# Kernel optimization log

Hardware: AMD Instinct MI355X
Metric: run time of the kernel (lower is better)

The kernel has to match this reference:

```python
import jax, jax.numpy as jnp
import numpy as np

EPS = 1e-6
H = 8        # num_heads
DH = 64      # head dim = embed_dim // num_heads
LN_EPS = 1e-5


def _layernorm(x, g, b):
    m = jnp.mean(x, axis=-1, keepdims=True)
    v = jnp.mean(jnp.square(x - m), axis=-1, keepdims=True)
    return (x - m) / jnp.sqrt(v + LN_EPS) * g + b


def _flow_attention(x, Wq, bq, Wk, bk, Wv, bv, Wo, bo):
    # Non-causal Flow-Attention (Flowformer): kernelized sigmoid Q/K,
    # flow-conservation sink/source normalization, linear-attention kv trick.
    B, L, D = x.shape
    S = L
    q = jax.nn.sigmoid((x @ Wq + bq).reshape(B, L, H, DH).transpose(0, 2, 1, 3))  # bhld
    k = jax.nn.sigmoid((x @ Wk + bk).reshape(B, S, H, DH).transpose(0, 2, 1, 3))
    v = (x @ Wv + bv).reshape(B, S, H, DH).transpose(0, 2, 1, 3)

    sink_incoming = 1.0 / jnp.einsum('nhld,nhd->nhl', q + EPS, k.sum(axis=2) + EPS)
    source_outgoing = 1.0 / jnp.einsum('nhld,nhd->nhl', k + EPS, q.sum(axis=2) + EPS)
    conserved_sink = jnp.einsum('nhld,nhd->nhl', q + EPS,
                                (k * source_outgoing[..., None]).sum(axis=2) + EPS)
    conserved_source = jnp.einsum('nhld,nhd->nhl', k + EPS,
                                  (q * sink_incoming[..., None]).sum(axis=2) + EPS)
    conserved_source = jnp.clip(conserved_source, -1.0, 1.0)
    sink_allocation = jax.nn.sigmoid(conserved_sink * (float(L) / float(S)))
    source_competition = jax.nn.softmax(conserved_source, axis=-1) * float(S)

    # linear attention: kv = k^T (v * comp), out = (q * sink_in) kv
    kv = jnp.einsum('nhld,nhlm->nhdm', k, v * source_competition[..., None])
    o = jnp.einsum('nhld,nhdm->nhlm', q * sink_incoming[..., None], kv)
    o = o * sink_allocation[..., None]
    o = o.transpose(0, 2, 1, 3).reshape(B, L, D)
    return o @ Wo + bo


def setup_inputs() -> dict:
    key = jax.random.key(0)
    ks = jax.random.split(key, 16)
    B, L, D, F = 2, 16384, 512, 2048
    s = 0.02
    inp = {
        'x': jax.random.normal(ks[0], (B, L, D), dtype=jnp.float32),
        'Wq': jax.random.normal(ks[1], (D, D), dtype=jnp.float32) * s,
        'bq': jnp.zeros((D,), jnp.float32),
        'Wk': jax.random.normal(ks[2], (D, D), dtype=jnp.float32) * s,
        'bk': jnp.zeros((D,), jnp.float32),
        'Wv': jax.random.normal(ks[3], (D, D), dtype=jnp.float32) * s,
        'bv': jnp.zeros((D,), jnp.float32),
        'Wo': jax.random.normal(ks[4], (D, D), dtype=jnp.float32) * s,
        'bo': jnp.zeros((D,), jnp.float32),
        'W1': jax.random.normal(ks[5], (D, F), dtype=jnp.float32) * s,
        'b1': jnp.zeros((F,), jnp.float32),
        'W2': jax.random.normal(ks[6], (F, D), dtype=jnp.float32) * s,
        'b2': jnp.zeros((D,), jnp.float32),
        'g1': jnp.ones((D,), jnp.float32),
        'be1': jnp.zeros((D,), jnp.float32),
        'g2': jnp.ones((D,), jnp.float32),
        'be2': jnp.zeros((D,), jnp.float32),
    }
    return inp


def reference(x, Wq, bq, Wk, bk, Wv, bv, Wo, bo, W1, b1, W2, b2, g1, be1, g2, be2):
    # norm_first FlowformerLayer. NOTE: original _sa_block returns
    # dropout(attn(x))[0, :, :] -> [L, D], broadcast-added over batch (faithful).
    sa = _flow_attention(_layernorm(x, g1, be1), Wq, bq, Wk, bk, Wv, bv, Wo, bo)[0]
    x = x + sa  # [B,L,D] + [L,D]
    h = _layernorm(x, g2, be2)
    h = jax.nn.gelu(h @ W1 + b1, approximate=False) @ W2 + b2
    return x + h
```

## Files before the change

### kernel.cpp

```cpp
#include <hip/hip_runtime.h>
#include <hip/hip_bf16.h>
#include <cstdint>
#include <cstddef>


#define L_SEQ 16384
#define EPSF 1e-6f

typedef __bf16 b16x8 __attribute__((ext_vector_type(8)));
typedef __bf16 b16x4 __attribute__((ext_vector_type(4)));
typedef float  f32x4 __attribute__((ext_vector_type(4)));

#define FENCE() asm volatile("" ::: "memory")
#define BARF()  { FENCE(); __builtin_amdgcn_s_barrier(); FENCE(); }
#define WAITV(n) asm volatile("s_waitcnt vmcnt(" #n ")" ::: "memory")

__device__ __forceinline__ void gload16(const void* g, void* l) {
  __builtin_amdgcn_global_load_lds((const __attribute__((address_space(1))) void*)g,
                                   (__attribute__((address_space(3))) void*)l, 16, 0, 0);
}

__device__ __forceinline__ float sigmoidf_(float x) { return 1.f / (1.f + __expf(-x)); }

__global__ __launch_bounds__(256) void convT(const float* __restrict__ src,
                                             __bf16* __restrict__ dst, int K, int N) {
  __shared__ float tile[32][33];
  const int k0 = blockIdx.y * 32, n0 = blockIdx.x * 32;
  const int tx = threadIdx.x & 31, ty = threadIdx.x >> 5;
#pragma unroll
  for (int i = 0; i < 32; i += 8) tile[ty + i][tx] = src[(size_t)(k0 + ty + i) * N + n0 + tx];
  __syncthreads();
#pragma unroll
  for (int i = 0; i < 32; i += 8)
    dst[(size_t)(n0 + ty + i) * K + k0 + tx] = (__bf16)tile[tx][ty + i];
}

__global__ __launch_bounds__(256) void biascat_k(const float* __restrict__ bq,
                                                 const float* __restrict__ bk,
                                                 const float* __restrict__ bv,
                                                 float* __restrict__ bc) {
  int i = blockIdx.x * 256 + threadIdx.x;
  bc[i] = (i < 512) ? bq[i] : (i < 1024) ? bk[i - 512] : bv[i - 1024];
}

__global__ __launch_bounds__(256) void zero_k(float* __restrict__ p, int n) {
  int i = blockIdx.x * 256 + threadIdx.x;
  if (i < n) p[i] = 0.f;
}

__global__ __launch_bounds__(128) void ln_rows(const float* __restrict__ x,
                                               const float* __restrict__ g,
                                               const float* __restrict__ be,
                                               __bf16* __restrict__ out) {
  const int row = blockIdx.x, t = threadIdx.x;
  const float4 xv = reinterpret_cast<const float4*>(x + (size_t)row * 512)[t];
  float s = xv.x + xv.y + xv.z + xv.w;
  float s2 = xv.x * xv.x + xv.y * xv.y + xv.z * xv.z + xv.w * xv.w;
#pragma unroll
  for (int off = 32; off > 0; off >>= 1) { s += __shfl_down(s, off); s2 += __shfl_down(s2, off); }
  __shared__ float red[4];
  if ((t & 63) == 0) { red[(t >> 6) * 2] = s; red[(t >> 6) * 2 + 1] = s2; }
  __syncthreads();
  const float S = red[0] + red[2], S2 = red[1] + red[3];
  const float mean = S * (1.f / 512.f);
  const float var = S2 * (1.f / 512.f) - mean * mean;
  const float inv = rsqrtf(var + 1e-5f);
  const float4 gv = reinterpret_cast<const float4*>(g)[t];
  const float4 bv = reinterpret_cast<const float4*>(be)[t];
  b16x4 o;
  o[0] = (__bf16)((xv.x - mean) * inv * gv.x + bv.x);
  o[1] = (__bf16)((xv.y - mean) * inv * gv.y + bv.y);
  o[2] = (__bf16)((xv.z - mean) * inv * gv.z + bv.z);
  o[3] = (__bf16)((xv.w - mean) * inv * gv.w + bv.w);
  reinterpret_cast<b16x4*>(out + (size_t)row * 512)[t] = o;
}

__global__ __launch_bounds__(128) void x2ln2_k(const float* __restrict__ x,
                                               const float* __restrict__ sa0,
                                               const float* __restrict__ sa1,
                                               const float* __restrict__ bo,
                                               const float* __restrict__ g,
                                               const float* __restrict__ be,
                                               float* __restrict__ xout,
                                               __bf16* __restrict__ lnout) {
  const int row = blockIdx.x, t = threadIdx.x;
  const int l = row & (L_SEQ - 1);
  float4 xv = reinterpret_cast<const float4*>(x + (size_t)row * 512)[t];
  const float4 s0 = reinterpret_cast<const float4*>(sa0 + (size_t)l * 512)[t];
  const float4 s1 = reinterpret_cast<const float4*>(sa1 + (size_t)l * 512)[t];
  const float4 bb = reinterpret_cast<const float4*>(bo)[t];
  xv.x += s0.x + s1.x + bb.x; xv.y += s0.y + s1.y + bb.y;
  xv.z += s0.z + s1.z + bb.z; xv.w += s0.w + s1.w + bb.w;
  reinterpret_cast<float4*>(xout + (size_t)row * 512)[t] = xv;
  float s = xv.x + xv.y + xv.z + xv.w;
  float s2 = xv.x * xv.x + xv.y * xv.y + xv.z * xv.z + xv.w * xv.w;
#pragma unroll
  for (int off = 32; off > 0; off >>= 1) { s += __shfl_down(s, off); s2 += __shfl_down(s2, off); }
  __shared__ float red[4];
  if ((t & 63) == 0) { red[(t >> 6) * 2] = s; red[(t >> 6) * 2 + 1] = s2; }
  __syncthreads();
  const float S = red[0] + red[2], S2 = red[1] + red[3];
  const float mean = S * (1.f / 512.f);
  const float var = S2 * (1.f / 512.f) - mean * mean;
  const float inv = rsqrtf(var + 1e-5f);
  const float4 gv = reinterpret_cast<const float4*>(g)[t];
  const float4 bv = reinterpret_cast<const float4*>(be)[t];
  b16x4 o;
  o[0] = (__bf16)((xv.x - mean) * inv * gv.x + bv.x);
  o[1] = (__bf16)((xv.y - mean) * inv * gv.y + bv.y);
  o[2] = (__bf16)((xv.z - mean) * inv * gv.z + bv.z);
  o[3] = (__bf16)((xv.w - mean) * inv * gv.w + bv.w);
  reinterpret_cast<b16x4*>(lnout + (size_t)row * 512)[t] = o;
}

template <int EPI, int KSPL>
__global__ __launch_bounds__(256, 4) void gemm128(const __bf16* __restrict__ A,
                                                  const __bf16* __restrict__ Bt,
                                                  const int M, const int N, const int K,
                                                  const float* __restrict__ bias,
                                                  float* __restrict__ f0,
                                                  __bf16* __restrict__ h0,
                                                  __bf16* __restrict__ h1,
                                                  float* __restrict__ f1,
                                                  float* __restrict__ f2) {
  __shared__ alignas(16) __bf16 lds[16384];

  if constexpr (KSPL) {
    const int z = blockIdx.y;
    A += (size_t)z * (K >> 1);
    Bt += (size_t)z * (K >> 1);
    f0 += (size_t)z * ((size_t)M * N);
  }
  const int nt = KSPL ? (K >> 6) : (K >> 5);

  const int nwg = gridDim.x;
  const int orig = blockIdx.x;
  const int cpx = nwg >> 3;
  const int wg = (orig & 7) * cpx + (orig >> 3);
  const int gx = N >> 7;
  const int bm = (wg / gx) << 7;
  const int bn = (wg % gx) << 7;

  const int t = threadIdx.x;
  const int w = t >> 6, lane = t & 63;
  const int wr = w >> 1, wc = w & 1;
  const int fr = lane & 15;
  const int kb = lane >> 4;

  const __bf16* As = A + (size_t)(bm + (t >> 2)) * K + (t & 3) * 8;
  const __bf16* Bs = Bt + (size_t)(bn + (t >> 2)) * K + (t & 3) * 8;

  f32x4 acc[4][4] = {};

  auto STG = [&](int s) {
    const int sel = (s & 1) * 4096;
    const __bf16* ap = As + (s << 5);
    const __bf16* bp = Bs + (s << 5);
    gload16(ap, &lds[sel + t * 8]);
    gload16(ap + (size_t)64 * K, &lds[sel + 2048 + t * 8]);
    gload16(bp, &lds[8192 + sel + t * 8]);
    gload16(bp + (size_t)64 * K, &lds[8192 + sel + 2048 + t * 8]);
  };

  STG(0);
  WAITV(0);
  BARF();

  for (int s = 0; s < nt; s++) {
    if (s + 1 < nt) STG(s + 1);
    const int ab = (s & 1) * 4096 + (wr * 64 + fr) * 32 + kb * 8;
    const int bb2 = 8192 + (s & 1) * 4096 + (wc * 64 + fr) * 32 + kb * 8;
    b16x8 av[4], bv[4];
#pragma unroll
    for (int m = 0; m < 4; m++)
      av[m] = *reinterpret_cast<const b16x8*>(&lds[ab + m * 512]);
#pragma unroll
    for (int n = 0; n < 4; n++)
      bv[n] = *reinterpret_cast<const b16x8*>(&lds[bb2 + n * 512]);
#pragma unroll
    for (int m = 0; m < 4; m++)
#pragma unroll
      for (int n = 0; n < 4; n++)
        acc[m][n] = __builtin_amdgcn_mfma_f32_16x16x32_bf16(av[m], bv[n], acc[m][n], 0, 0, 0);
    WAITV(0);
    BARF();
  }

  const int r0 = kb * 4;
  const int cc = fr;
  if constexpr (EPI == 0) {
    const int which = bn >> 9;
    float cs[4] = {0.f, 0.f, 0.f, 0.f};
#pragma unroll
    for (int m = 0; m < 4; m++) {
#pragma unroll
      for (int n = 0; n < 4; n++) {
        const int col = bn + wc * 64 + n * 16 + cc;
        const int c2 = col & 511;
#pragma unroll
        for (int r = 0; r < 4; r++) {
          const int row = bm + wr * 64 + m * 16 + r0 + r;
          float val = acc[m][n][r] + bias[col];
          if (which < 2) {
            val = sigmoidf_(val);
            cs[n] += val;
            ((which == 0) ? h0 : h1)[(size_t)row * 512 + c2] = (__bf16)val;
          } else {
            f0[(size_t)row * 512 + c2] = val;
          }
        }
      }
    }
    if (which < 2) {
      float* sums = (which == 0) ? f1 : f2;
#pragma unroll
      for (int n = 0; n < 4; n++) {
        float s = cs[n];
        s += __shfl_xor(s, 16);
        s += __shfl_xor(s, 32);
        if (kb == 0) atomicAdd(&sums[(bn & 511) + wc * 64 + n * 16 + cc], s);
      }
    }
  } else {
#pragma unroll
    for (int m = 0; m < 4; m++) {
#pragma unroll
      for (int n = 0; n < 4; n++) {
        const int col = bn + wc * 64 + n * 16 + cc;
#pragma unroll
        for (int r = 0; r < 4; r++) {
          const int row = bm + wr * 64 + m * 16 + r0 + r;
          float val = acc[m][n][r];
          if constexpr (EPI == 1) {
            f0[(size_t)row * N + col] = val;
          } else if constexpr (EPI == 2) {
            const float xg = val + bias[col];
            const float gel = 0.5f * xg * (1.f + erff(xg * 0.70710678118f));
            h0[(size_t)row * N + col] = (__bf16)gel;
          } else {
            const size_t idx = (size_t)row * N + col;
            f0[idx] = f0[idx] + val + bias[col];
          }
        }
      }
    }
  }
}

__global__ __launch_bounds__(256) void attn_pass1(const __bf16* __restrict__ q,
                                                  const __bf16* __restrict__ k,
                                                  const float* __restrict__ qsum,
                                                  const float* __restrict__ ksum,
                                                  float* __restrict__ si_out,
                                                  float* __restrict__ qkpart) {
  __shared__ float lsQ[512], lsK[512];
  const int t = threadIdx.x, lane = t & 63, wv = t >> 6;
  const int c0 = lane * 8;
  lsQ[t] = 0.f; lsQ[t + 256] = 0.f;
  lsK[t] = 0.f; lsK[t + 256] = 0.f;
  __syncthreads();
  float qs[8], ks[8];
#pragma unroll
  for (int j = 0; j < 8; j++) {
    qs[j] = qsum[c0 + j] + EPSF;
    ks[j] = ksum[c0 + j] + EPSF;
  }
  const int h = lane >> 3;
  float qacc[8] = {}, kacc[8] = {};
#pragma unroll 1
  for (int i = 0; i < 8; i++) {
    const int l = blockIdx.x * 32 + wv * 8 + i;
    const b16x8 q8 = *reinterpret_cast<const b16x8*>(q + (size_t)l * 512 + c0);
    const b16x8 k8 = *reinterpret_cast<const b16x8*>(k + (size_t)l * 512 + c0);
    float qf[8], kf[8];
    float p1 = 0.f, p2 = 0.f;
#pragma unroll
    for (int j = 0; j < 8; j++) {
      qf[j] = (float)q8[j]; kf[j] = (float)k8[j];
      p1 += (qf[j] + EPSF) * ks[j];
      p2 += (kf[j] + EPSF) * qs[j];
    }
    p1 += __shfl_xor(p1, 1); p2 += __shfl_xor(p2, 1);
    p1 += __shfl_xor(p1, 2); p2 += __shfl_xor(p2, 2);
    p1 += __shfl_xor(p1, 4); p2 += __shfl_xor(p2, 4);
    const float siv = 1.f / p1, sov = 1.f / p2;
    if ((lane & 7) == 0) si_out[h * L_SEQ + l] = siv;
#pragma unroll
    for (int j = 0; j < 8; j++) { qacc[j] += qf[j] * siv; kacc[j] += kf[j] * sov; }
  }
#pragma unroll
  for (int j = 0; j < 8; j++) {
    atomicAdd(&lsQ[c0 + j], qacc[j]);
    atomicAdd(&lsK[c0 + j], kacc[j]);
  }
  __syncthreads();
  float* qp = qkpart + (size_t)blockIdx.x * 1024;
  qp[t] = lsQ[t];
  qp[t + 256] = lsQ[t + 256];
  qp[t + 512] = lsK[t];
  qp[t + 768] = lsK[t + 256];
}

__global__ __launch_bounds__(256) void reduce_qk(const float* __restrict__ qkpart,
                                                 float* __restrict__ outv) {
  const int i = blockIdx.x * 256 + threadIdx.x;
  float s = 0.f;
#pragma unroll 4
  for (int b = 0; b < 512; b++) s += qkpart[(size_t)b * 1024 + i];
  outv[i] = s;
}

__global__ __launch_bounds__(256) void kv_part(const __bf16* __restrict__ k,
                                               const float* __restrict__ v,
                                               const float* __restrict__ qsi,
                                               float* __restrict__ kvpart,
                                               float* __restrict__ separt) {
  const int h = blockIdx.y, bx = blockIdx.x, t = threadIdx.x;
  __shared__ float lsK[64 * 68];
  __shared__ float lsV[64 * 68];
  __shared__ float lsRed[256];
  const int r = t >> 2, cq = (t & 3) * 16;
  float qv[16];
#pragma unroll
  for (int j = 0; j < 16; j++) qv[j] = qsi[h * 64 + cq + j] + EPSF;
  const int d = t & 63, mg = t >> 6;
  f32x4 acc4[4] = {};
  float seloc = 0.f;
#pragma unroll 1
  for (int sc = 0; sc < 4; sc++) {
    const int l = bx * 256 + sc * 64 + r;
    __syncthreads();
    const b16x8 k8a = *reinterpret_cast<const b16x8*>(k + (size_t)l * 512 + h * 64 + cq);
    const b16x8 k8b = *reinterpret_cast<const b16x8*>(k + (size_t)l * 512 + h * 64 + cq + 8);
    f32x4 v4[4];
#pragma unroll
    for (int jj = 0; jj < 4; jj++)
      v4[jj] = *reinterpret_cast<const f32x4*>(v + (size_t)l * 512 + h * 64 + cq + jj * 4);
    float kf[16];
#pragma unroll
    for (int j = 0; j < 8; j++) { kf[j] = (float)k8a[j]; kf[8 + j] = (float)k8b[j]; }
    float p = 0.f;
#pragma unroll
    for (int j = 0; j < 16; j++) p += (kf[j] + EPSF) * qv[j];
    p += __shfl_xor(p, 1);
    p += __shfl_xor(p, 2);
    p = fminf(fmaxf(p, -1.f), 1.f);
    const float ce = __expf(p);
    if ((t & 3) == 0) seloc += ce;
#pragma unroll
    for (int j = 0; j < 16; j++) lsK[r * 68 + cq + j] = kf[j];
#pragma unroll
    for (int jj = 0; jj < 4; jj++)
      *reinterpret_cast<f32x4*>(&lsV[r * 68 + cq + jj * 4]) = v4[jj] * ce;
    __syncthreads();
    for (int rr = 0; rr < 64; rr++) {
      const float kd = lsK[rr * 68 + d];
      const f32x4* lv = reinterpret_cast<const f32x4*>(&lsV[rr * 68 + mg * 16]);
#pragma unroll
      for (int jj = 0; jj < 4; jj++) acc4[jj] += lv[jj] * kd;
    }
  }
  float* kp = kvpart + ((size_t)h * 64 + bx) * 4096;
#pragma unroll
  for (int jj = 0; jj < 4; jj++)
    *reinterpret_cast<f32x4*>(&kp[d * 64 + mg * 16 + jj * 4]) = acc4[jj];
  lsRed[t] = ((t & 3) == 0) ? seloc : 0.f;
  __syncthreads();
  for (int s2 = 128; s2 > 0; s2 >>= 1) {
    if (t < s2) lsRed[t] += lsRed[t + s2];
    __syncthreads();
  }
  if (t == 0) separt[h * 64 + bx] = lsRed[0];
}

__global__ __launch_bounds__(256) void kv_reduce(const float* __restrict__ kvpart,
                                                 const float* __restrict__ separt,
                                                 float* __restrict__ kvout,
                                                 float* __restrict__ sumexp) {
  const int h = blockIdx.y, t = threadIdx.x;
  const int i = blockIdx.x * 256 + t;
  float s = 0.f;
#pragma unroll 4
  for (int b = 0; b < 64; b++) s += kvpart[((size_t)h * 64 + b) * 4096 + i];
  kvout[h * 4096 + i] = s;
  if (blockIdx.x == 0 && t < 64) {
    float e = separt[h * 64 + t];
#pragma unroll
    for (int off2 = 32; off2 > 0; off2 >>= 1) e += __shfl_down(e, off2);
    if (t == 0) sumexp[h] = e;
  }
}

__global__ __launch_bounds__(256) void o_kernel(const __bf16* __restrict__ q,
                                                const float* __restrict__ kvin,
                                                const float* __restrict__ si,
                                                const float* __restrict__ kso,
                                                const float* __restrict__ sumexp,
                                                __bf16* __restrict__ o) {
  const int h = blockIdx.y;
  const int l0 = blockIdx.x * 32;
  const int t = threadIdx.x;
  __shared__ float lsKV[64 * 64];
  __shared__ float lsQ[32 * 65];
  __shared__ float lsF[32];
  const float Sfac = (float)L_SEQ / sumexp[h];
#pragma unroll
  for (int j = 0; j < 16; j++) lsKV[t + j * 256] = kvin[h * 4096 + t + j * 256];
  const int r = t >> 3, c8 = (t & 7) * 8;
  float ksov[8];
#pragma unroll
  for (int j = 0; j < 8; j++) ksov[j] = kso[h * 64 + c8 + j] + EPSF;
  const b16x8 q8 = *reinterpret_cast<const b16x8*>(q + (size_t)(l0 + r) * 512 + h * 64 + c8);
  float p = 0.f;
#pragma unroll
  for (int j = 0; j < 8; j++) {
    const float qf = (float)q8[j];
    lsQ[r * 65 + c8 + j] = qf;
    p += (qf + EPSF) * ksov[j];
  }
  p += __shfl_xor(p, 1);
  p += __shfl_xor(p, 2);
  p += __shfl_xor(p, 4);
  if ((t & 7) == 0) lsF[r] = sigmoidf_(p) * si[h * L_SEQ + l0 + r] * Sfac;
  __syncthreads();
  const int m = t & 63, rg = t >> 6;
#pragma unroll 1
  for (int i = 0; i < 8; i++) {
    const int rr = rg + i * 4;
    float a = 0.f;
#pragma unroll
    for (int dd = 0; dd < 64; dd++) a += lsQ[rr * 65 + dd] * lsKV[dd * 64 + m];
    o[(size_t)(l0 + rr) * 512 + h * 64 + m] = (__bf16)(a * lsF[rr]);
  }
}

extern "C" void kernel_launch(void* const* d_in, const int* in_sizes, int n_in,
                              void* d_out, int out_size, void* d_ws, size_t ws_size,
                              hipStream_t stream) {
  const float* x  = (const float*)d_in[0];
  const float* Wq = (const float*)d_in[1];
  const float* bq = (const float*)d_in[2];
  const float* Wk = (const float*)d_in[3];
  const float* bk = (const float*)d_in[4];
  const float* Wv = (const float*)d_in[5];
  const float* bv = (const float*)d_in[6];
  const float* Wo = (const float*)d_in[7];
  const float* bo = (const float*)d_in[8];
  const float* W1 = (const float*)d_in[9];
  const float* b1 = (const float*)d_in[10];
  const float* W2 = (const float*)d_in[11];
  const float* b2 = (const float*)d_in[12];
  const float* g1 = (const float*)d_in[13];
  const float* be1 = (const float*)d_in[14];
  const float* g2 = (const float*)d_in[15];
  const float* be2 = (const float*)d_in[16];
  float* out = (float*)d_out;

  char* ws = (char*)d_ws;
  size_t off = 0;
  auto alloc = [&](size_t bytes) -> char* {
    char* p = ws + off;
    off += (bytes + 255) & ~(size_t)255;
    return p;
  };

  char* regA = alloc(134217728);
  __bf16* ln1  = (__bf16*)regA;
  __bf16* qb16 = (__bf16*)(regA + 16777216);
  __bf16* kb16 = (__bf16*)(regA + 33554432);
  float*  vb   = (float*)(regA + 50331648);
  __bf16* ob   = (__bf16*)(regA + 83886080);
  float*  sa   = (float*)regA;
  __bf16* act  = (__bf16*)regA;

  __bf16* ln2 = (__bf16*)alloc((size_t)32768 * 512 * 2);
  __bf16* Wqkvt = (__bf16*)alloc((size_t)1536 * 512 * 2);
  __bf16* Wot = (__bf16*)alloc((size_t)512 * 512 * 2);
  __bf16* W1t = (__bf16*)alloc((size_t)2048 * 512 * 2);
  __bf16* W2t = (__bf16*)alloc((size_t)512 * 2048 * 2);
  float* biascat = (float*)alloc(1536 * 4);
  float* si = (float*)alloc((size_t)8 * L_SEQ * 4);
  float* stats = (float*)alloc(34880 * 4);
  float* qsum = stats;
  float* ksum = stats + 512;
  float* qsi = stats + 1024;
  float* kso = stats + 1536;
  float* sumexp = stats + 2048;
  float* kvbuf = stats + 2112;
  float* kvpart = (float*)alloc((size_t)8 * 64 * 4096 * 4);
  float* separt = (float*)alloc(512 * 4);
  float* qkpart = (float*)alloc((size_t)512 * 1024 * 4);

  convT<<<dim3(16, 16), 256, 0, stream>>>(Wq, Wqkvt, 512, 512);
  convT<<<dim3(16, 16), 256, 0, stream>>>(Wk, Wqkvt + (size_t)512 * 512, 512, 512);
  convT<<<dim3(16, 16), 256, 0, stream>>>(Wv, Wqkvt + (size_t)1024 * 512, 512, 512);
  convT<<<dim3(16, 16), 256, 0, stream>>>(Wo, Wot, 512, 512);
  convT<<<dim3(64, 16), 256, 0, stream>>>(W1, W1t, 512, 2048);
  convT<<<dim3(16, 64), 256, 0, stream>>>(W2, W2t, 2048, 512);
  biascat_k<<<6, 256, 0, stream>>>(bq, bk, bv, biascat);
  zero_k<<<(2112 + 255) / 256, 256, 0, stream>>>(stats, 2112);

  ln_rows<<<L_SEQ, 128, 0, stream>>>(x, g1, be1, ln1);
  gemm128<0, 0><<<1536, 256, 0, stream>>>(ln1, Wqkvt, L_SEQ, 1536, 512,
                                          biascat, vb, qb16, kb16, qsum, ksum);

  attn_pass1<<<512, 256, 0, stream>>>(qb16, kb16, qsum, ksum, si, qkpart);
  reduce_qk<<<4, 256, 0, stream>>>(qkpart, qsi);
  kv_part<<<dim3(64, 8), 256, 0, stream>>>(kb16, vb, qsi, kvpart, separt);
  kv_reduce<<<dim3(16, 8), 256, 0, stream>>>(kvpart, separt, kvbuf, sumexp);
  o_kernel<<<dim3(L_SEQ / 32, 8), 256, 0, stream>>>(qb16, kvbuf, si, kso, sumexp, ob);

  gemm128<1, 1><<<dim3(512, 2), 256, 0, stream>>>(ob, Wot, L_SEQ, 512, 512,
                                                  nullptr, sa, nullptr, nullptr,
                                                  nullptr, nullptr);

  x2ln2_k<<<2 * L_SEQ, 128, 0, stream>>>(x, sa, sa + (size_t)L_SEQ * 512, bo,
                                         g2, be2, out, ln2);

  gemm128<2, 0><<<4096, 256, 0, stream>>>(ln2, W1t, 2 * L_SEQ, 2048, 512,
                                          b1, nullptr, act, nullptr, nullptr, nullptr);
  gemm128<3, 0><<<1024, 256, 0, stream>>>(act, W2t, 2 * L_SEQ, 512, 2048,
                                          b2, out, nullptr, nullptr, nullptr, nullptr);
}
```

Measured before the change: 514.0 us.

## Store V projection in bf16 and merge weight-prep kernels into one launch

Merges the six weight transpose/convert launches, the bias concat and the stats zeroing into a single prep kernel that dispatches on block index. This cuts launch overhead. It also stores the V projection as bf16 instead of fp32, halving the V write in the QKV GEMM epilogue and the V read in kv_part. The trade-off is lower precision on V before the kv accumulation, plus scalar LDS stores in kv_part where f32x4 stores were used before.

```diff
diff --git a/kernel.cpp b/kernel.cpp
--- a/kernel.cpp
+++ b/kernel.cpp
@@ -22,10 +22,39 @@
 
 __device__ __forceinline__ float sigmoidf_(float x) { return 1.f / (1.f + __expf(-x)); }
 
-__global__ __launch_bounds__(256) void convT(const float* __restrict__ src,
-                                             __bf16* __restrict__ dst, int K, int N) {
+__global__ __launch_bounds__(256) void prep_k(const float* __restrict__ Wq,
+                                              const float* __restrict__ Wk,
+                                              const float* __restrict__ Wv,
+                                              const float* __restrict__ Wo,
+                                              const float* __restrict__ W1,
+                                              const float* __restrict__ W2,
+                                              const float* __restrict__ bq,
+                                              const float* __restrict__ bk,
+                                              const float* __restrict__ bv,
+                                              __bf16* __restrict__ Wqkvt,
+                                              __bf16* __restrict__ Wot,
+                                              __bf16* __restrict__ W1t,
+                                              __bf16* __restrict__ W2t,
+                                              float* __restrict__ biascat,
+                                              float* __restrict__ zstats) {
+  const int b = blockIdx.x;
+  if (b >= 3072) {
+    const int i = (b - 3072) * 256 + threadIdx.x;
+    if (i < 1536) biascat[i] = (i < 512) ? bq[i] : (i < 1024) ? bk[i - 512] : bv[i - 1024];
+    else if (i < 1536 + 2112) zstats[i - 1536] = 0.f;
+    return;
+  }
+  const float* src;
+  __bf16* dst;
+  int K, N, bx, by;
+  if (b < 256)       { src = Wq; dst = Wqkvt;                      K = 512;  N = 512;  const int r = b;        bx = r & 15; by = r >> 4; }
+  else if (b < 512)  { src = Wk; dst = Wqkvt + (size_t)512 * 512;  K = 512;  N = 512;  const int r = b - 256;  bx = r & 15; by = r >> 4; }
+  else if (b < 768)  { src = Wv; dst = Wqkvt + (size_t)1024 * 512; K = 512;  N = 512;  const int r = b - 512;  bx = r & 15; by = r >> 4; }
+  else if (b < 1024) { src = Wo; dst = Wot;                        K = 512;  N = 512;  const int r = b - 768;  bx = r & 15; by = r >> 4; }
+  else if (b < 2048) { src = W1; dst = W1t;                        K = 512;  N = 2048; const int r = b - 1024; bx = r & 63; by = r >> 6; }
+  else               { src = W2; dst = W2t;                        K = 2048; N = 512;  const int r = b - 2048; bx = r & 15; by = r >> 4; }
   __shared__ float tile[32][33];
-  const int k0 = blockIdx.y * 32, n0 = blockIdx.x * 32;
+  const int k0 = by * 32, n0 = bx * 32;
   const int tx = threadIdx.x & 31, ty = threadIdx.x >> 5;
 #pragma unroll
   for (int i = 0; i < 32; i += 8) tile[ty + i][tx] = src[(size_t)(k0 + ty + i) * N + n0 + tx];
@@ -33,19 +62,6 @@
 #pragma unroll
   for (int i = 0; i < 32; i += 8)
     dst[(size_t)(n0 + ty + i) * K + k0 + tx] = (__bf16)tile[tx][ty + i];
-}
-
-__global__ __launch_bounds__(256) void biascat_k(const float* __restrict__ bq,
-                                                 const float* __restrict__ bk,
-                                                 const float* __restrict__ bv,
-                                                 float* __restrict__ bc) {
-  int i = blockIdx.x * 256 + threadIdx.x;
-  bc[i] = (i < 512) ? bq[i] : (i < 1024) ? bk[i - 512] : bv[i - 1024];
-}
-
-__global__ __launch_bounds__(256) void zero_k(float* __restrict__ p, int n) {
-  int i = blockIdx.x * 256 + threadIdx.x;
-  if (i < n) p[i] = 0.f;
 }
 
 __global__ __launch_bounds__(128) void ln_rows(const float* __restrict__ x,
@@ -206,7 +222,7 @@
             cs[n] += val;
             ((which == 0) ? h0 : h1)[(size_t)row * 512 + c2] = (__bf16)val;
           } else {
-            f0[(size_t)row * 512 + c2] = val;
+            ((__bf16*)f0)[(size_t)row * 512 + c2] = (__bf16)val;
           }
         }
       }
@@ -230,7 +246,7 @@
 #pragma unroll
         for (int r = 0; r < 4; r++) {
           const int row = bm + wr * 64 + m * 16 + r0 + r;
-          float val = acc[m][n][r];
+          const float val = acc[m][n][r];
           if constexpr (EPI == 1) {
             f0[(size_t)row * N + col] = val;
           } else if constexpr (EPI == 2) {
@@ -311,7 +327,7 @@
 }
 
 __global__ __launch_bounds__(256) void kv_part(const __bf16* __restrict__ k,
-                                               const float* __restrict__ v,
+                                               const __bf16* __restrict__ v,
                                                const float* __restrict__ qsi,
                                                float* __restrict__ kvpart,
                                                float* __restrict__ separt) {
@@ -332,13 +348,14 @@
     __syncthreads();
     const b16x8 k8a = *reinterpret_cast<const b16x8*>(k + (size_t)l * 512 + h * 64 + cq);
     const b16x8 k8b = *reinterpret_cast<const b16x8*>(k + (size_t)l * 512 + h * 64 + cq + 8);
-    f32x4 v4[4];
-#pragma unroll
-    for (int jj = 0; jj < 4; jj++)
-      v4[jj] = *reinterpret_cast<const f32x4*>(v + (size_t)l * 512 + h * 64 + cq + jj * 4);
-    float kf[16];
-#pragma unroll
-    for (int j = 0; j < 8; j++) { kf[j] = (float)k8a[j]; kf[8 + j] = (float)k8b[j]; }
+    const b16x8 v8a = *reinterpret_cast<const b16x8*>(v + (size_t)l * 512 + h * 64 + cq);
+    const b16x8 v8b = *reinterpret_cast<const b16x8*>(v + (size_t)l * 512 + h * 64 + cq + 8);
+    float kf[16], vf[16];
+#pragma unroll
+    for (int j = 0; j < 8; j++) {
+      kf[j] = (float)k8a[j]; kf[8 + j] = (float)k8b[j];
+      vf[j] = (float)v8a[j]; vf[8 + j] = (float)v8b[j];
+    }
     float p = 0.f;
 #pragma unroll
     for (int j = 0; j < 16; j++) p += (kf[j] + EPSF) * qv[j];
@@ -348,10 +365,10 @@
     const float ce = __expf(p);
     if ((t & 3) == 0) seloc += ce;
 #pragma unroll
-    for (int j = 0; j < 16; j++) lsK[r * 68 + cq + j] = kf[j];
-#pragma unroll
-    for (int jj = 0; jj < 4; jj++)
-      *reinterpret_cast<f32x4*>(&lsV[r * 68 + cq + jj * 4]) = v4[jj] * ce;
+    for (int j = 0; j < 16; j++) {
+      lsK[r * 68 + cq + j] = kf[j];
+      lsV[r * 68 + cq + j] = vf[j] * ce;
+    }
     __syncthreads();
     for (int rr = 0; rr < 64; rr++) {
       const float kd = lsK[rr * 68 + d];
@@ -468,7 +485,7 @@
   __bf16* ln1  = (__bf16*)regA;
   __bf16* qb16 = (__bf16*)(regA + 16777216);
   __bf16* kb16 = (__bf16*)(regA + 33554432);
-  float*  vb   = (float*)(regA + 50331648);
+  __bf16* vb16 = (__bf16*)(regA + 50331648);
   __bf16* ob   = (__bf16*)(regA + 83886080);
   float*  sa   = (float*)regA;
   __bf16* act  = (__bf16*)regA;
@@ -491,22 +508,16 @@
   float* separt = (float*)alloc(512 * 4);
   float* qkpart = (float*)alloc((size_t)512 * 1024 * 4);
 
-  convT<<<dim3(16, 16), 256, 0, stream>>>(Wq, Wqkvt, 512, 512);
-  convT<<<dim3(16, 16), 256, 0, stream>>>(Wk, Wqkvt + (size_t)512 * 512, 512, 512);
-  convT<<<dim3(16, 16), 256, 0, stream>>>(Wv, Wqkvt + (size_t)1024 * 512, 512, 512);
-  convT<<<dim3(16, 16), 256, 0, stream>>>(Wo, Wot, 512, 512);
-  convT<<<dim3(64, 16), 256, 0, stream>>>(W1, W1t, 512, 2048);
-  convT<<<dim3(16, 64), 256, 0, stream>>>(W2, W2t, 2048, 512);
-  biascat_k<<<6, 256, 0, stream>>>(bq, bk, bv, biascat);
-  zero_k<<<(2112 + 255) / 256, 256, 0, stream>>>(stats, 2112);
+  prep_k<<<3087, 256, 0, stream>>>(Wq, Wk, Wv, Wo, W1, W2, bq, bk, bv,
+                                   Wqkvt, Wot, W1t, W2t, biascat, stats);
 
   ln_rows<<<L_SEQ, 128, 0, stream>>>(x, g1, be1, ln1);
   gemm128<0, 0><<<1536, 256, 0, stream>>>(ln1, Wqkvt, L_SEQ, 1536, 512,
-                                          biascat, vb, qb16, kb16, qsum, ksum);
+                                          biascat, (float*)vb16, qb16, kb16, qsum, ksum);
 
   attn_pass1<<<512, 256, 0, stream>>>(qb16, kb16, qsum, ksum, si, qkpart);
   reduce_qk<<<4, 256, 0, stream>>>(qkpart, qsi);
-  kv_part<<<dim3(64, 8), 256, 0, stream>>>(kb16, vb, qsi, kvpart, separt);
+  kv_part<<<dim3(64, 8), 256, 0, stream>>>(kb16, vb16, qsi, kvpart, separt);
   kv_reduce<<<dim3(16, 8), 256, 0, stream>>>(kvpart, separt, kvbuf, sumexp);
   o_kernel<<<dim3(L_SEQ / 32, 8), 256, 0, stream>>>(qb16, kvbuf, si, kso, sumexp, ob);
 
```

New measurement: 498.7 us. -3.0%, faster.
